# Kernel optimization log

Hardware: AMD Instinct MI355X
Metric: run time of the kernel (lower is better)

Reference implementation:

```python
import jax, jax.numpy as jnp
import numpy as np

# Model dims
H = 1024          # hidden_size
I = 2048          # intermediate_size
E = 8             # num_experts
IE = I // E       # expert_intermediate_size = 256
V = 100000        # vocab_size
B, S = 8, 2048


def _rowwise_quantize(x):
    """Dynamic per-row int8 quantization (faithful to dynamic_quantize_int8, per_channel=True).
    Returns quantized values kept in float32 (identical values to int8->float cast) and per-row scale."""
    max_vals = jnp.max(jnp.abs(x), axis=-1, keepdims=True)
    scale = jnp.maximum(max_vals / 127.0, 1e-8)
    x_q = jnp.clip(jnp.round(x / scale), -128.0, 127.0)
    return x_q, scale[..., 0]


def _quantize_weight(w):
    """Per-output-channel int8 quantization of a [K, N] weight (as in from_float)."""
    max_vals = jnp.max(jnp.abs(w), axis=0, keepdims=True)      # [1, N]
    scale = jnp.maximum(max_vals / 127.0, 1e-8)
    w_q = jnp.clip(jnp.round(w / scale), -128.0, 127.0).astype(jnp.int8)
    return w_q, scale[0]


def setup_inputs() -> dict:
    key = jax.random.key(0)
    ks = jax.random.split(key, 6)
    hidden_states = jax.random.normal(ks[0], (B, S, H), dtype=jnp.float32)
    token_ids = jax.random.randint(ks[1], (B, S), 0, V, dtype=jnp.int32)

    # Pre-quantized expert weights (int8) with per-output-channel fp32 scales.
    gate_w = jax.random.normal(ks[2], (E, H, IE), dtype=jnp.float32) * 0.02
    up_w = jax.random.normal(ks[3], (E, H, IE), dtype=jnp.float32) * 0.02
    down_w = jax.random.normal(ks[4], (E, IE, H), dtype=jnp.float32) * 0.02
    gate_q, gate_scale = jax.vmap(_quantize_weight)(gate_w)   # [E,H,IE] int8, [E,IE]
    up_q, up_scale = jax.vmap(_quantize_weight)(up_w)         # [E,H,IE] int8, [E,IE]
    down_q, down_scale = jax.vmap(_quantize_weight)(down_w)   # [E,IE,H] int8, [E,H]

    # Deterministic contiguous token->expert mapping (V divisible by E here).
    token_to_expert = jnp.minimum(jnp.arange(V, dtype=jnp.int32) // (V // E), E - 1)

    return {
        "hidden_states": hidden_states,
        "token_ids": token_ids,
        "gate_q": gate_q, "gate_scale": gate_scale,
        "up_q": up_q, "up_scale": up_scale,
        "down_q": down_q, "down_scale": down_scale,
        "token_to_expert": token_to_expert,
    }


def reference(hidden_states, token_ids, gate_q, gate_scale, up_q, up_scale,
              down_q, down_scale, token_to_expert):
    Bh, Sh, Hh = hidden_states.shape
    n_exp = gate_q.shape[0]
    vocab = token_to_expert.shape[0]

    tid = jnp.clip(token_ids, 0, vocab - 1)
    expert_ids = token_to_expert[tid].reshape(-1)             # [T]

    x = hidden_states.reshape(-1, Hh)                          # [T, H]
    # Per-row activation quantization is expert-independent -> do it once for all tokens.
    x_q, x_s = _rowwise_quantize(x)                            # [T,H], [T]

    gq = gate_q.astype(jnp.float32)
    uq = up_q.astype(jnp.float32)
    dq = down_q.astype(jnp.float32)

    out = jnp.zeros_like(x)
    for e in range(n_exp):  # small fixed expert count
        # fused quantize-GEMM: int8 matmul + per-row activation scale + per-col weight scale
        gate = (x_q @ gq[e]) * x_s[:, None] * gate_scale[e][None, :]   # [T, IE]
        up = (x_q @ uq[e]) * x_s[:, None] * up_scale[e][None, :]       # [T, IE]
        inter = jax.nn.silu(gate) * up
        i_q, i_s = _rowwise_quantize(inter)
        o = (i_q @ dq[e]) * i_s[:, None] * down_scale[e][None, :]      # [T, H]
        out = jnp.where((expert_ids == e)[:, None], o, out)
    return out.reshape(Bh, Sh, Hh)
```

## Files before the change

### kernel.cpp

```cpp
#include <hip/hip_runtime.h>

typedef int   int4v   __attribute__((ext_vector_type(4)));
typedef float float4v __attribute__((ext_vector_type(4)));

#define T_TOK 16384
#define HD    1024
#define IE    256
#define EN    8
#define VSZ   100000

#define M_OFF 16
#define M_TS1 25

#define XQ_OFF   0ull
#define PB1_OFF  21053440ull
#define PB2_OFF  25247744ull
#define PERM_OFF 27344896ull
#define XS_OFF   27410688ull
#define META_OFF 27542272ull

__device__ __forceinline__ void gload16(const void* g, void* l) {
    __builtin_amdgcn_global_load_lds(
        (const __attribute__((address_space(1))) unsigned int*)g,
        (__attribute__((address_space(3))) unsigned int*)l,
        16, 0, 0);
}

__global__ __launch_bounds__(1024) void k_route(const int* __restrict__ ids,
                                                const int* __restrict__ t2e,
                                                int* __restrict__ perm,
                                                int* __restrict__ meta) {
    __shared__ int lbase[1024][EN];
    __shared__ int wsum[16][EN];
    __shared__ int goff[EN], tot[EN];
    const int tid = threadIdx.x, lane = tid & 63, wv = tid >> 6;

    #pragma unroll
    for (int e = 0; e < EN; ++e) lbase[tid][e] = 0;
    int e_of[16];
    #pragma unroll
    for (int i = 0; i < 16; ++i) {
        int id = ids[tid * 16 + i];
        id = min(max(id, 0), VSZ - 1);
        int e = t2e[id];
        e_of[i] = e;
        lbase[tid][e]++;
    }
    #pragma unroll
    for (int e = 0; e < EN; ++e) {
        int v = lbase[tid][e];
        int inc = v;
        #pragma unroll
        for (int s = 1; s < 64; s <<= 1) {
            int u = __shfl_up(inc, s, 64);
            if (lane >= s) inc += u;
        }
        lbase[tid][e] = inc - v;
        if (lane == 63) wsum[wv][e] = inc;
    }
    __syncthreads();
    if (tid < EN) {
        int run = 0;
        for (int w2 = 0; w2 < 16; ++w2) { int t = wsum[w2][tid]; wsum[w2][tid] = run; run += t; }
        tot[tid] = run;
    }
    __syncthreads();
    if (tid == 0) {
        int off = 0, t1 = 0;
        meta[M_OFF] = 0; meta[M_TS1] = 0;
        #pragma unroll
        for (int e = 0; e < EN; ++e) {
            goff[e] = off;
            off += tot[e];
            t1 += (tot[e] + 63) >> 6;
            meta[M_OFF + e + 1] = off;
            meta[M_TS1 + e + 1] = t1;
        }
    }
    __syncthreads();
    #pragma unroll
    for (int i = 0; i < 16; ++i) {
        int e = e_of[i];
        int c = lbase[tid][e];
        lbase[tid][e] = c + 1;
        perm[goff[e] + wsum[wv][e] + c] = tid * 16 + i;
    }
}

__global__ __launch_bounds__(256) void k_pre(const float* __restrict__ hidden,
                                             const int* __restrict__ gq,
                                             const int* __restrict__ uq,
                                             const int* __restrict__ dq,
                                             signed char* __restrict__ xq,
                                             float* __restrict__ xs,
                                             signed char* __restrict__ pb1,
                                             signed char* __restrict__ pb2) {
    int b = blockIdx.x;
    if (b < 4096) {
        int w = threadIdx.x >> 6, lane = threadIdx.x & 63;
        int token = (b << 2) + w;
        const float* row = hidden + (size_t)token * HD;
        float v[16];
        #pragma unroll
        for (int j = 0; j < 4; ++j) {
            float4v f = *(const float4v*)(row + lane * 16 + j * 4);
            v[j*4+0] = f[0]; v[j*4+1] = f[1]; v[j*4+2] = f[2]; v[j*4+3] = f[3];
        }
        float mx = 0.0f;
        #pragma unroll
        for (int j = 0; j < 16; ++j) mx = fmaxf(mx, fabsf(v[j]));
        #pragma unroll
        for (int s = 1; s < 64; s <<= 1) mx = fmaxf(mx, __shfl_xor(mx, s, 64));
        float sc = fmaxf(mx / 127.0f, 1e-8f);
        if (lane == 0) xs[token] = sc;
        int4v pk;
        #pragma unroll
        for (int j = 0; j < 4; ++j) {
            int bb[4];
            #pragma unroll
            for (int u = 0; u < 4; ++u) {
                float t = rintf(v[j*4+u] / sc);
                t = fminf(fmaxf(t, -128.0f), 127.0f);
                bb[u] = (int)t;
            }
            pk[j] = (bb[0] & 255) | ((bb[1] & 255) << 8) | ((bb[2] & 255) << 16) | (bb[3] << 24);
        }
        *(int4v*)(xq + (size_t)token * HD + lane * 16) = pk;
    } else {
        int idx = (b - 4096) * 256 + threadIdx.x;
        if (idx < 262144) {
            int n = idx & 511, kc = (idx >> 9) & 63, e = idx >> 15;
            const int* src = (n < 256) ? gq + (((size_t)((e << 10) + (kc << 4)) << 8) + n)
                                       : uq + (((size_t)((e << 10) + (kc << 4)) << 8) + (n - 256));
            int4v pk;
            #pragma unroll
            for (int jj = 0; jj < 4; ++jj) {
                int b0 = src[(size_t)(jj * 4 + 0) << 8], b1 = src[(size_t)(jj * 4 + 1) << 8];
                int b2 = src[(size_t)(jj * 4 + 2) << 8], b3 = src[(size_t)(jj * 4 + 3) << 8];
                pk[jj] = (b0 & 255) | ((b1 & 255) << 8) | ((b2 & 255) << 16) | (b3 << 24);
            }
            *(int4v*)(pb1 + ((size_t)((((e << 6) + kc) << 9) + n) << 4)) = pk;
        } else {
            int j = idx - 262144;
            int n = j & 1023, kc = (j >> 10) & 15, e = j >> 14;
            const int* src = dq + (((size_t)((e << 8) + (kc << 4)) << 10) + n);
            int4v pk;
            #pragma unroll
            for (int jj = 0; jj < 4; ++jj) {
                int b0 = src[(size_t)(jj * 4 + 0) << 10], b1 = src[(size_t)(jj * 4 + 1) << 10];
                int b2 = src[(size_t)(jj * 4 + 2) << 10], b3 = src[(size_t)(jj * 4 + 3) << 10];
                pk[jj] = (b0 & 255) | ((b1 & 255) << 8) | ((b2 & 255) << 16) | (b3 << 24);
            }
            *(int4v*)(pb2 + ((size_t)((((e << 4) + kc) << 10) + n) << 4)) = pk;
        }
    }
}

__global__ __launch_bounds__(256, 2) void k_mlp(const signed char* __restrict__ xq,
                                                const signed char* __restrict__ pb1,
                                                const signed char* __restrict__ pb2,
                                                const float* __restrict__ xs,
                                                const float* __restrict__ gsc,
                                                const float* __restrict__ usc,
                                                const float* __restrict__ dsc,
                                                const int* __restrict__ meta,
                                                const int* __restrict__ perm,
                                                float* __restrict__ out) {
    int b = blockIdx.x;
    int e = -1, m0 = 0, gend = 0;
    #pragma unroll
    for (int i = 0; i < EN; ++i) {
        int s0 = meta[M_TS1 + i], s1 = meta[M_TS1 + i + 1];
        if (b >= s0 && b < s1) { e = i; m0 = meta[M_OFF + i] + ((b - s0) << 6); gend = meta[M_OFF + i + 1]; }
    }
    if (e < 0) return;
    const int w = threadIdx.x >> 6, lane = threadIdx.x & 63;
    const int q = lane >> 4, r = lane & 15;

    __shared__ __align__(16) signed char lB[2][32768];
    __shared__ __align__(16) signed char arena[16384];
    float* pmax = (float*)(arena + 8192);
    float* rsc  = (float*)(arena + 9216);
    int*   ptok = (int*)(arena + 9472);

    if (threadIdx.x < 64) ptok[threadIdx.x] = perm[min(m0 + (int)threadIdx.x, T_TOK - 1)];
    __syncthreads();

    int tokr[4][4];
    #pragma unroll
    for (int mi = 0; mi < 4; ++mi)
        #pragma unroll
        for (int g = 0; g < 4; ++g)
            tokr[mi][g] = ptok[(mi << 4) + (q << 2) + g];

    const signed char* pbe1 = pb1 + (size_t)e * (64 * 512 * 16);
    const signed char* pbe2 = pb2 + (size_t)e * (16 * 1024 * 16);
    const int arow = (w << 4) + (lane >> 2);
    const int acq  = (lane & 3) ^ ((lane >> 2) & 3);
    const signed char* ga_base = xq + (size_t)ptok[arow] * HD + (acq << 4);

    #define G1_STAGE(buf, kt)                                                          \
        {                                                                              \
            int kc0 = (kt) << 2;                                                       \
            _Pragma("unroll")                                                          \
            for (int j = 0; j < 8; ++j) {                                              \
                int n = ((j << 6) + lane) ^ ((w & 1) << 3);                            \
                gload16(pbe1 + (((size_t)(kc0 + w) * 512 + n) << 4),                   \
                        &lB[buf][((w << 3) + j) << 10]);                               \
            }                                                                          \
            gload16(ga_base + ((kt) << 6), arena + ((buf) << 12) + (w << 10));         \
        }

    #define G2_STAGE(buf, st)                                                          \
        {                                                                              \
            int kc0 = ((st) & 3) << 2; int nhs = (st) >> 2;                            \
            _Pragma("unroll")                                                          \
            for (int j = 0; j < 8; ++j) {                                              \
                int n = ((j << 6) + lane) ^ ((w & 1) << 3);                            \
                gload16(pbe2 + (((size_t)(kc0 + w) * 1024 + (nhs << 9) + n) << 4),     \
                        &lB[buf][((w << 3) + j) << 10]);                               \
            }                                                                          \
        }

    int4v zero = {0, 0, 0, 0};
    int4v accg[4][4], accu[4][4];
    #pragma unroll
    for (int mi = 0; mi < 4; ++mi)
        #pragma unroll
        for (int i = 0; i < 4; ++i) { accg[mi][i] = zero; accu[mi][i] = zero; }

    G1_STAGE(0, 0);
    for (int kt = 0; kt < 16; ++kt) {
        int cur = kt & 1;
        if (kt < 15) G1_STAGE(cur ^ 1, kt + 1);
        __syncthreads();
        int4v a[4];
        #pragma unroll
        for (int mi = 0; mi < 4; ++mi)
            a[mi] = *(const int4v*)&arena[(cur << 12) + ((((mi << 4) + r) << 6) + ((q ^ (r & 3)) << 4))];
        #pragma unroll
        for (int i = 0; i < 4; ++i) {
            int n = (w << 6) + (i << 4) + r;
            int sg = (q << 9) + (n ^ ((q & 1) << 3));
            int su = (q << 9) + ((n + 256) ^ ((q & 1) << 3));
            int4v bg = *(const int4v*)&lB[cur][sg << 4];
            int4v bu = *(const int4v*)&lB[cur][su << 4];
            #pragma unroll
            for (int mi = 0; mi < 4; ++mi) {
                accg[mi][i] = __builtin_amdgcn_mfma_i32_16x16x64_i8(a[mi], bg, accg[mi][i], 0, 0, 0);
                accu[mi][i] = __builtin_amdgcn_mfma_i32_16x16x64_i8(a[mi], bu, accu[mi][i], 0, 0, 0);
            }
        }
        __syncthreads();
    }
    #undef G1_STAGE

    G2_STAGE(0, 0);

    float gs[4], us[4];
    #pragma unroll
    for (int i = 0; i < 4; ++i) {
        int n = (w << 6) + (i << 4) + r;
        gs[i] = gsc[e * IE + n];
        us[i] = usc[e * IE + n];
    }
    float xsr[4][4];
    #pragma unroll
    for (int mi = 0; mi < 4; ++mi)
        #pragma unroll
        for (int g = 0; g < 4; ++g)
            xsr[mi][g] = xs[tokr[mi][g]];

    float inter[4][4][4];
    float pm[4][4];
    #pragma unroll
    for (int mi = 0; mi < 4; ++mi)
        #pragma unroll
        for (int g = 0; g < 4; ++g) {
            float mx = 0.0f;
            #pragma unroll
            for (int i = 0; i < 4; ++i) {
                float gv = (float)accg[mi][i][g] * xsr[mi][g] * gs[i];
                float uv = (float)accu[mi][i][g] * xsr[mi][g] * us[i];
                float sg = gv / (1.0f + expf(-gv));
                float vv = sg * uv;
                inter[mi][i][g] = vv;
                mx = fmaxf(mx, fabsf(vv));
            }
            #pragma unroll
            for (int s = 1; s < 16; s <<= 1) mx = fmaxf(mx, __shfl_xor(mx, s, 64));
            pm[mi][g] = mx;
        }

    if (r == 0) {
        #pragma unroll
        for (int mi = 0; mi < 4; ++mi)
            #pragma unroll
            for (int g = 0; g < 4; ++g)
                pmax[(w << 6) + (mi << 4) + (q << 2) + g] = pm[mi][g];
    }
    __syncthreads();
    if (threadIdx.x < 64) {
        int row = threadIdx.x;
        float mx = fmaxf(fmaxf(pmax[row], pmax[64 + row]), fmaxf(pmax[128 + row], pmax[192 + row]));
        rsc[row] = fmaxf(mx / 127.0f, 1e-8f);
    }
    __syncthreads();
    float rscr[4][4];
    #pragma unroll
    for (int mi = 0; mi < 4; ++mi)
        #pragma unroll
        for (int g = 0; g < 4; ++g)
            rscr[mi][g] = rsc[(mi << 4) + (q << 2) + g];
    __syncthreads();

    #pragma unroll
    for (int mi = 0; mi < 4; ++mi)
        #pragma unroll
        for (int g = 0; g < 4; ++g) {
            int row = (mi << 4) + (q << 2) + g;
            float sc = rscr[mi][g];
            #pragma unroll
            for (int i = 0; i < 4; ++i) {
                float t = rintf(inter[mi][i][g] / sc);
                t = fminf(fmaxf(t, -128.0f), 127.0f);
                arena[(row << 8) + ((((w << 2) + i) ^ (row & 3)) << 4) + r] = (signed char)(int)t;
            }
        }

    int4v acc2[4][8];
    for (int st = 0; st < 8; ++st) {
        int cur = st & 1;
        if (st < 7) G2_STAGE(cur ^ 1, st + 1);
        if ((st & 3) == 0) {
            #pragma unroll
            for (int mi = 0; mi < 4; ++mi)
                #pragma unroll
                for (int i = 0; i < 8; ++i) acc2[mi][i] = zero;
        }
        __syncthreads();
        int4v a2[4];
        #pragma unroll
        for (int mi = 0; mi < 4; ++mi) {
            int row2 = (mi << 4) + r;
            a2[mi] = *(const int4v*)&arena[(row2 << 8) + (((((st & 3) << 2) + q) ^ (r & 3)) << 4)];
        }
        #pragma unroll
        for (int i = 0; i < 8; ++i) {
            int n = (w << 7) + (i << 4) + r;
            int sb = (q << 9) + (n ^ ((q & 1) << 3));
            int4v bb = *(const int4v*)&lB[cur][sb << 4];
            #pragma unroll
            for (int mi = 0; mi < 4; ++mi)
                acc2[mi][i] = __builtin_amdgcn_mfma_i32_16x16x64_i8(a2[mi], bb, acc2[mi][i], 0, 0, 0);
        }
        if ((st & 3) == 3) {
            int nhs = st >> 2;
            float ds[8];
            #pragma unroll
            for (int i = 0; i < 8; ++i)
                ds[i] = dsc[e * HD + (nhs << 9) + (w << 7) + (i << 4) + r];
            #pragma unroll
            for (int mi = 0; mi < 4; ++mi)
                #pragma unroll
                for (int g = 0; g < 4; ++g) {
                    int slot = m0 + (mi << 4) + (q << 2) + g;
                    if (slot < gend) {
                        size_t ob = (size_t)tokr[mi][g] * HD + (nhs << 9) + (w << 7) + r;
                        #pragma unroll
                        for (int i = 0; i < 8; ++i)
                            out[ob + (i << 4)] = (float)acc2[mi][i][g] * rscr[mi][g] * ds[i];
                    }
                }
        }
        __syncthreads();
    }
    #undef G2_STAGE
}

extern "C" void kernel_launch(void* const* d_in, const int* in_sizes, int n_in,
                              void* d_out, int out_size, void* d_ws, size_t ws_size,
                              hipStream_t stream) {
    const float* hidden = (const float*)d_in[0];
    const int*   ids    = (const int*)d_in[1];
    const int*   gq     = (const int*)d_in[2];
    const float* gsc    = (const float*)d_in[3];
    const int*   uq     = (const int*)d_in[4];
    const float* usc    = (const float*)d_in[5];
    const int*   dq     = (const int*)d_in[6];
    const float* dsc    = (const float*)d_in[7];
    const int*   t2e    = (const int*)d_in[8];
    float* out = (float*)d_out;

    char* ws = (char*)d_ws;
    signed char* xq  = (signed char*)(ws + XQ_OFF);
    signed char* pb1 = (signed char*)(ws + PB1_OFF);
    signed char* pb2 = (signed char*)(ws + PB2_OFF);
    int*   perm = (int*)(ws + PERM_OFF);
    float* xs   = (float*)(ws + XS_OFF);
    int*   meta = (int*)(ws + META_OFF);

    k_route<<<1, 1024, 0, stream>>>(ids, t2e, perm, meta);
    k_pre<<<5632, 256, 0, stream>>>(hidden, gq, uq, dq, xq, xs, pb1, pb2);
    k_mlp<<<264, 256, 0, stream>>>(xq, pb1, pb2, xs, gsc, usc, dsc, meta, perm, out);
}
```

Measured before the change: 233.8 us.

## Split routing into multi-block hist/scan/assign and halve MLP token tile to 32

Replaces the single-block routing kernel with a three-kernel histogram, scan and atomic-assign pipeline spread over 64 blocks. The MLP kernel tile drops from 64 to 32 tokens per block, so 520 blocks are launched instead of 264, and a block-index remap interleaves the experts. One barrier per pipeline stage is removed by moving the sync before the prefetch. This gives better CU occupancy and a shorter serial routing step, at the cost of re-reading each expert's weights twice as often per token and two extra launches. The atomic assignment also makes token order within an expert nondeterministic.

```diff
diff --git a/kernel.cpp b/kernel.cpp
--- a/kernel.cpp
+++ b/kernel.cpp
@@ -18,6 +18,8 @@
 #define PERM_OFF 27344896ull
 #define XS_OFF   27410688ull
 #define META_OFF 27542272ull
+#define BC_OFF   27542528ull
+#define BB_OFF   27544576ull
 
 __device__ __forceinline__ void gload16(const void* g, void* l) {
     __builtin_amdgcn_global_load_lds(
@@ -26,65 +28,61 @@
         16, 0, 0);
 }
 
-__global__ __launch_bounds__(1024) void k_route(const int* __restrict__ ids,
-                                                const int* __restrict__ t2e,
-                                                int* __restrict__ perm,
-                                                int* __restrict__ meta) {
-    __shared__ int lbase[1024][EN];
-    __shared__ int wsum[16][EN];
-    __shared__ int goff[EN], tot[EN];
-    const int tid = threadIdx.x, lane = tid & 63, wv = tid >> 6;
-
-    #pragma unroll
-    for (int e = 0; e < EN; ++e) lbase[tid][e] = 0;
-    int e_of[16];
-    #pragma unroll
-    for (int i = 0; i < 16; ++i) {
-        int id = ids[tid * 16 + i];
-        id = min(max(id, 0), VSZ - 1);
-        int e = t2e[id];
-        e_of[i] = e;
-        lbase[tid][e]++;
-    }
-    #pragma unroll
-    for (int e = 0; e < EN; ++e) {
-        int v = lbase[tid][e];
-        int inc = v;
-        #pragma unroll
-        for (int s = 1; s < 64; s <<= 1) {
-            int u = __shfl_up(inc, s, 64);
-            if (lane >= s) inc += u;
-        }
-        lbase[tid][e] = inc - v;
-        if (lane == 63) wsum[wv][e] = inc;
-    }
-    __syncthreads();
-    if (tid < EN) {
-        int run = 0;
-        for (int w2 = 0; w2 < 16; ++w2) { int t = wsum[w2][tid]; wsum[w2][tid] = run; run += t; }
-        tot[tid] = run;
-    }
-    __syncthreads();
-    if (tid == 0) {
+__global__ void k_hist(const int* __restrict__ ids, const int* __restrict__ t2e,
+                       int* __restrict__ bc) {
+    __shared__ int h[EN];
+    if (threadIdx.x < EN) h[threadIdx.x] = 0;
+    __syncthreads();
+    int t = blockIdx.x * 256 + threadIdx.x;
+    int id = ids[t]; id = min(max(id, 0), VSZ - 1);
+    atomicAdd(&h[t2e[id]], 1);
+    __syncthreads();
+    if (threadIdx.x < EN) bc[blockIdx.x * EN + threadIdx.x] = h[threadIdx.x];
+}
+
+__global__ __launch_bounds__(512) void k_scan(const int* __restrict__ bc,
+                                              int* __restrict__ bbase,
+                                              int* __restrict__ meta) {
+    int e = threadIdx.x >> 6;
+    int b = threadIdx.x & 63;
+    int c = bc[b * EN + e];
+    int inc = c;
+    #pragma unroll
+    for (int s = 1; s < 64; s <<= 1) {
+        int v = __shfl_up(inc, s, 64);
+        if (b >= s) inc += v;
+    }
+    int exc = inc - c;
+    __shared__ int tot[EN];
+    __shared__ int goff[EN];
+    if (b == 63) tot[e] = inc;
+    __syncthreads();
+    if (threadIdx.x == 0) {
         int off = 0, t1 = 0;
         meta[M_OFF] = 0; meta[M_TS1] = 0;
         #pragma unroll
-        for (int e = 0; e < EN; ++e) {
-            goff[e] = off;
-            off += tot[e];
-            t1 += (tot[e] + 63) >> 6;
-            meta[M_OFF + e + 1] = off;
-            meta[M_TS1 + e + 1] = t1;
-        }
-    }
-    __syncthreads();
-    #pragma unroll
-    for (int i = 0; i < 16; ++i) {
-        int e = e_of[i];
-        int c = lbase[tid][e];
-        lbase[tid][e] = c + 1;
-        perm[goff[e] + wsum[wv][e] + c] = tid * 16 + i;
-    }
+        for (int i = 0; i < EN; ++i) {
+            goff[i] = off;
+            int cc = tot[i];
+            off += cc; t1 += (cc + 31) >> 5;
+            meta[M_OFF + i + 1] = off;
+            meta[M_TS1 + i + 1] = t1;
+        }
+    }
+    __syncthreads();
+    bbase[b * EN + e] = goff[e] + exc;
+}
+
+__global__ void k_assign(const int* __restrict__ ids, const int* __restrict__ t2e,
+                         const int* __restrict__ bbase, int* __restrict__ perm) {
+    __shared__ int cur[EN];
+    if (threadIdx.x < EN) cur[threadIdx.x] = bbase[blockIdx.x * EN + threadIdx.x];
+    __syncthreads();
+    int t = blockIdx.x * 256 + threadIdx.x;
+    int id = ids[t]; id = min(max(id, 0), VSZ - 1);
+    int e = t2e[id];
+    int slot = atomicAdd(&cur[e], 1);
+    perm[slot] = t;
 }
 
 __global__ __launch_bounds__(256) void k_pre(const float* __restrict__ hidden,
@@ -166,29 +164,29 @@
                                                 const int* __restrict__ meta,
                                                 const int* __restrict__ perm,
                                                 float* __restrict__ out) {
-    int b = blockIdx.x;
+    int b = (blockIdx.x & 7) * 65 + (blockIdx.x >> 3);
     int e = -1, m0 = 0, gend = 0;
     #pragma unroll
     for (int i = 0; i < EN; ++i) {
         int s0 = meta[M_TS1 + i], s1 = meta[M_TS1 + i + 1];
-        if (b >= s0 && b < s1) { e = i; m0 = meta[M_OFF + i] + ((b - s0) << 6); gend = meta[M_OFF + i + 1]; }
+        if (b >= s0 && b < s1) { e = i; m0 = meta[M_OFF + i] + ((b - s0) << 5); gend = meta[M_OFF + i + 1]; }
     }
     if (e < 0) return;
     const int w = threadIdx.x >> 6, lane = threadIdx.x & 63;
     const int q = lane >> 4, r = lane & 15;
 
     __shared__ __align__(16) signed char lB[2][32768];
-    __shared__ __align__(16) signed char arena[16384];
-    float* pmax = (float*)(arena + 8192);
-    float* rsc  = (float*)(arena + 9216);
-    int*   ptok = (int*)(arena + 9472);
-
-    if (threadIdx.x < 64) ptok[threadIdx.x] = perm[min(m0 + (int)threadIdx.x, T_TOK - 1)];
-    __syncthreads();
-
-    int tokr[4][4];
-    #pragma unroll
-    for (int mi = 0; mi < 4; ++mi)
+    __shared__ __align__(16) signed char arena[8192];
+    float* pmax = (float*)(arena + 4096);
+    float* rsc  = (float*)(arena + 4608);
+    int*   ptok = (int*)(arena + 4736);
+
+    if (threadIdx.x < 32) ptok[threadIdx.x] = perm[min(m0 + (int)threadIdx.x, T_TOK - 1)];
+    __syncthreads();
+
+    int tokr[2][4];
+    #pragma unroll
+    for (int mi = 0; mi < 2; ++mi)
         #pragma unroll
         for (int g = 0; g < 4; ++g)
             tokr[mi][g] = ptok[(mi << 4) + (q << 2) + g];
@@ -197,7 +195,7 @@
     const signed char* pbe2 = pb2 + (size_t)e * (16 * 1024 * 16);
     const int arow = (w << 4) + (lane >> 2);
     const int acq  = (lane & 3) ^ ((lane >> 2) & 3);
-    const signed char* ga_base = xq + (size_t)ptok[arow] * HD + (acq << 4);
+    const signed char* ga_base = xq + (size_t)ptok[arow & 31] * HD + (acq << 4);
 
     #define G1_STAGE(buf, kt)                                                          \
         {                                                                              \
@@ -208,7 +206,7 @@
                 gload16(pbe1 + (((size_t)(kc0 + w) * 512 + n) << 4),                   \
                         &lB[buf][((w << 3) + j) << 10]);                               \
             }                                                                          \
-            gload16(ga_base + ((kt) << 6), arena + ((buf) << 12) + (w << 10));         \
+            if (w < 2) gload16(ga_base + ((kt) << 6), arena + ((buf) << 11) + (w << 10)); \
         }
 
     #define G2_STAGE(buf, st)                                                          \
@@ -223,21 +221,21 @@
         }
 
     int4v zero = {0, 0, 0, 0};
-    int4v accg[4][4], accu[4][4];
-    #pragma unroll
-    for (int mi = 0; mi < 4; ++mi)
+    int4v accg[2][4], accu[2][4];
+    #pragma unroll
+    for (int mi = 0; mi < 2; ++mi)
         #pragma unroll
         for (int i = 0; i < 4; ++i) { accg[mi][i] = zero; accu[mi][i] = zero; }
 
     G1_STAGE(0, 0);
     for (int kt = 0; kt < 16; ++kt) {
         int cur = kt & 1;
+        __syncthreads();
         if (kt < 15) G1_STAGE(cur ^ 1, kt + 1);
-        __syncthreads();
-        int4v a[4];
-        #pragma unroll
-        for (int mi = 0; mi < 4; ++mi)
-            a[mi] = *(const int4v*)&arena[(cur << 12) + ((((mi << 4) + r) << 6) + ((q ^ (r & 3)) << 4))];
+        int4v a[2];
+        #pragma unroll
+        for (int mi = 0; mi < 2; ++mi)
+            a[mi] = *(const int4v*)&arena[(cur << 11) + ((((mi << 4) + r) << 6) + ((q ^ (r & 3)) << 4))];
         #pragma unroll
         for (int i = 0; i < 4; ++i) {
             int n = (w << 6) + (i << 4) + r;
@@ -246,12 +244,11 @@
             int4v bg = *(const int4v*)&lB[cur][sg << 4];
             int4v bu = *(const int4v*)&lB[cur][su << 4];
             #pragma unroll
-            for (int mi = 0; mi < 4; ++mi) {
+            for (int mi = 0; mi < 2; ++mi) {
                 accg[mi][i] = __builtin_amdgcn_mfma_i32_16x16x64_i8(a[mi], bg, accg[mi][i], 0, 0, 0);
                 accu[mi][i] = __builtin_amdgcn_mfma_i32_16x16x64_i8(a[mi], bu, accu[mi][i], 0, 0, 0);
             }
         }
-        __syncthreads();
     }
     #undef G1_STAGE
 
@@ -264,17 +261,17 @@
         gs[i] = gsc[e * IE + n];
         us[i] = usc[e * IE + n];
     }
-    float xsr[4][4];
-    #pragma unroll
-    for (int mi = 0; mi < 4; ++mi)
+    float xsr[2][4];
+    #pragma unroll
+    for (int mi = 0; mi < 2; ++mi)
         #pragma unroll
         for (int g = 0; g < 4; ++g)
             xsr[mi][g] = xs[tokr[mi][g]];
 
-    float inter[4][4][4];
-    float pm[4][4];
-    #pragma unroll
-    for (int mi = 0; mi < 4; ++mi)
+    float inter[2][4][4];
+    float pm[2][4];
+    #pragma unroll
+    for (int mi = 0; mi < 2; ++mi)
         #pragma unroll
         for (int g = 0; g < 4; ++g) {
             float mx = 0.0f;
@@ -292,30 +289,31 @@
             pm[mi][g] = mx;
         }
 
+    __syncthreads();
     if (r == 0) {
         #pragma unroll
-        for (int mi = 0; mi < 4; ++mi)
+        for (int mi = 0; mi < 2; ++mi)
             #pragma unroll
             for (int g = 0; g < 4; ++g)
-                pmax[(w << 6) + (mi << 4) + (q << 2) + g] = pm[mi][g];
-    }
-    __syncthreads();
-    if (threadIdx.x < 64) {
+                pmax[(w << 5) + (mi << 4) + (q << 2) + g] = pm[mi][g];
+    }
+    __syncthreads();
+    if (threadIdx.x < 32) {
         int row = threadIdx.x;
-        float mx = fmaxf(fmaxf(pmax[row], pmax[64 + row]), fmaxf(pmax[128 + row], pmax[192 + row]));
+        float mx = fmaxf(fmaxf(pmax[row], pmax[32 + row]), fmaxf(pmax[64 + row], pmax[96 + row]));
         rsc[row] = fmaxf(mx / 127.0f, 1e-8f);
     }
     __syncthreads();
-    float rscr[4][4];
-    #pragma unroll
-    for (int mi = 0; mi < 4; ++mi)
+    float rscr[2][4];
+    #pragma unroll
+    for (int mi = 0; mi < 2; ++mi)
         #pragma unroll
         for (int g = 0; g < 4; ++g)
             rscr[mi][g] = rsc[(mi << 4) + (q << 2) + g];
     __syncthreads();
 
     #pragma unroll
-    for (int mi = 0; mi < 4; ++mi)
+    for (int mi = 0; mi < 2; ++mi)
         #pragma unroll
         for (int g = 0; g < 4; ++g) {
             int row = (mi << 4) + (q << 2) + g;
@@ -328,20 +326,20 @@
             }
         }
 
-    int4v acc2[4][8];
+    int4v acc2[2][8];
     for (int st = 0; st < 8; ++st) {
         int cur = st & 1;
+        __syncthreads();
         if (st < 7) G2_STAGE(cur ^ 1, st + 1);
         if ((st & 3) == 0) {
             #pragma unroll
-            for (int mi = 0; mi < 4; ++mi)
+            for (int mi = 0; mi < 2; ++mi)
                 #pragma unroll
                 for (int i = 0; i < 8; ++i) acc2[mi][i] = zero;
         }
-        __syncthreads();
-        int4v a2[4];
-        #pragma unroll
-        for (int mi = 0; mi < 4; ++mi) {
+        int4v a2[2];
+        #pragma unroll
+        for (int mi = 0; mi < 2; ++mi) {
             int row2 = (mi << 4) + r;
             a2[mi] = *(const int4v*)&arena[(row2 << 8) + (((((st & 3) << 2) + q) ^ (r & 3)) << 4)];
         }
@@ -351,7 +349,7 @@
             int sb = (q << 9) + (n ^ ((q & 1) << 3));
             int4v bb = *(const int4v*)&lB[cur][sb << 4];
             #pragma unroll
-            for (int mi = 0; mi < 4; ++mi)
+            for (int mi = 0; mi < 2; ++mi)
                 acc2[mi][i] = __builtin_amdgcn_mfma_i32_16x16x64_i8(a2[mi], bb, acc2[mi][i], 0, 0, 0);
         }
         if ((st & 3) == 3) {
@@ -361,7 +359,7 @@
             for (int i = 0; i < 8; ++i)
                 ds[i] = dsc[e * HD + (nhs << 9) + (w << 7) + (i << 4) + r];
             #pragma unroll
-            for (int mi = 0; mi < 4; ++mi)
+            for (int mi = 0; mi < 2; ++mi)
                 #pragma unroll
                 for (int g = 0; g < 4; ++g) {
                     int slot = m0 + (mi << 4) + (q << 2) + g;
@@ -373,7 +371,6 @@
                     }
                 }
         }
-        __syncthreads();
     }
     #undef G2_STAGE
 }
@@ -399,8 +396,12 @@
     int*   perm = (int*)(ws + PERM_OFF);
     float* xs   = (float*)(ws + XS_OFF);
     int*   meta = (int*)(ws + META_OFF);
-
-    k_route<<<1, 1024, 0, stream>>>(ids, t2e, perm, meta);
+    int*   bc   = (int*)(ws + BC_OFF);
+    int*   bbase= (int*)(ws + BB_OFF);
+
+    k_hist<<<64, 256, 0, stream>>>(ids, t2e, bc);
+    k_scan<<<1, 512, 0, stream>>>(bc, bbase, meta);
+    k_assign<<<64, 256, 0, stream>>>(ids, t2e, bbase, perm);
     k_pre<<<5632, 256, 0, stream>>>(hidden, gq, uq, dq, xq, xs, pb1, pb2);
-    k_mlp<<<264, 256, 0, stream>>>(xq, pb1, pb2, xs, gsc, usc, dsc, meta, perm, out);
-}
+    k_mlp<<<520, 256, 0, stream>>>(xq, pb1, pb2, xs, gsc, usc, dsc, meta, perm, out);
+}
```

Measured after the change: 204.6 us. 1.14x faster.
